# Kernel tuning notes

Hardware: AMD Instinct MI355X
Metric: run time of the kernel (lower is better)

## Reference

```python
import jax, jax.numpy as jnp
import numpy as np
from math import comb

N_VARS = 4

def _binom_vec(n):
    return jnp.asarray([comb(n, i) for i in range(n + 1)], dtype=jnp.float32)

def _conv_ind(L):
    M = np.zeros((L, L, 2 * L - 1), dtype=np.float32)
    for i in range(L):
        for j in range(L):
            M[i, j, i + j] = 1.0
    return jnp.asarray(M)

def _elev(d, D):
    # Bernstein degree-elevation matrix (d+1, D+1)
    E = np.zeros((d + 1, D + 1), dtype=np.float32)
    for k in range(D + 1):
        for i in range(d + 1):
            if 0 <= k - i <= D - d:
                E[i, k] = comb(d, i) * comb(D - d, k - i) / comb(D, k)
    return jnp.asarray(E)

def _mult_const(p, c):
    # multiply implicit-Bernstein poly (T, n, L) by scalar c: scale variable-0 rows
    return jnp.concatenate([p[:, :1, :] * c, p[:, 1:, :]], axis=1)

def _const_term(c, n, L):
    return _mult_const(jnp.ones((1, n, L), dtype=jnp.float32), c)

def _square_poly(p):
    # Bernstein product of p with itself: (T,n,L) -> (T*T, n, 2L-1)
    T, n, L = p.shape
    w = p * _binom_vec(L - 1)
    conv = jnp.einsum('avi,bvj,ijk->abvk', w, w, _conv_ind(L))
    return (conv / _binom_vec(2 * L - 2)).reshape(T * T, n, 2 * L - 1)

def _ibf_minmax(p):
    # interval bound of IBF poly: per-row min/max, interval product over vars, sum over terms
    lo = p.min(axis=2); hi = p.max(axis=2)  # (T, n)
    L_, U_ = lo[:, 0], hi[:, 0]
    for v in range(1, p.shape[1]):
        c = jnp.stack([L_ * lo[:, v], L_ * hi[:, v], U_ * lo[:, v], U_ * hi[:, v]])
        L_, U_ = c.min(axis=0), c.max(axis=0)
    return L_.sum(), U_.sum()

def _quad_of_poly(p, coeffs):
    # a*p^2 + b*p + c in implicit Bernstein form; degree doubles
    T, n, L = p.shape
    a, b, c = coeffs[0], coeffs[1], coeffs[2]
    p2 = _mult_const(_square_poly(p), a)
    bp = jnp.einsum('tvi,ik->tvk', _mult_const(p, b), _elev(L - 1, 2 * L - 2))
    return jnp.concatenate([p2, bp, _const_term(c, n, 2 * L - 1)], axis=0)

def _combine(inputs, weights):
    # sum_k w_k * P_k: scale each poly's var-0 rows by w_k, concatenate terms
    s = jnp.concatenate([inputs[:, :, :1, :] * weights[:, None, None, None],
                         inputs[:, :, 1:, :]], axis=2)
    K, T, n, L = s.shape
    return s.reshape(K * T, n, L)

def setup_inputs():
    key = jax.random.key(0)
    ks = jax.random.split(key, 5)
    K, T, n, L = 32, 16, N_VARS, 4
    return {
        'layer_inputs_under': 0.1 * jax.random.normal(ks[0], (K, T * n, L), jnp.float32),
        'layer_inputs_over': 0.1 * jax.random.normal(ks[1], (K, T * n, L), jnp.float32),
        'layer_inputs_under_degrees': jnp.full((K, n), L - 1, jnp.int32),
        'layer_inputs_over_degrees': jnp.full((K, n), L - 1, jnp.int32),
        'node_pos_weights': jax.random.normal(ks[2], (K,), jnp.float32),
        'node_neg_weights': jax.random.normal(ks[3], (K,), jnp.float32),
        'node_bias': 0.1 * jax.random.normal(ks[4], (1,), jnp.float32),
    }

def reference(layer_inputs_under, layer_inputs_over, layer_inputs_under_degrees,
              layer_inputs_over_degrees, node_pos_weights, node_neg_weights, node_bias):
    n = N_VARS
    K, TN, L = layer_inputs_under.shape
    T = TN // n
    iu = layer_inputs_under.reshape(K, T, n, L)
    io = layer_inputs_over.reshape(K, T, n, L)
    bias = node_bias[0]
    under = jnp.concatenate([_combine(io, node_neg_weights),
                             _combine(iu, node_pos_weights),
                             _const_term(bias, n, L)], axis=0)
    over = jnp.concatenate([_combine(io, node_pos_weights),
                            _combine(iu, node_neg_weights),
                            _const_term(bias, n, L)], axis=0)
    deg = jnp.maximum(layer_inputs_under_degrees.max(axis=0),
                      layer_inputs_over_degrees.max(axis=0)).astype(jnp.float32)
    l = _ibf_minmax(under)[0]
    u = _ibf_minmax(over)[1]
    lf, uf = float(l), float(u)
    L2 = 2 * L - 1
    if uf <= 0.0:  # node always inactive
        z = jnp.zeros((1,), jnp.float32)
        return z, z, jnp.zeros(n, jnp.float32), jnp.zeros(n, jnp.float32)
    if lf >= 0.0:  # node always active -> identity
        return under.reshape(-1, L), over.reshape(-1, L), deg, deg
    # l < 0 < u: quadratic ReLU relaxation (degree doubles)
    # under: (x^2 - l*x)/(u-l) <= relu(x); over: u*(x-l)^2/(u-l)^2 >= relu(x)
    cu = jnp.stack([1.0 / (u - l), -l / (u - l), jnp.zeros_like(u)])
    co = jnp.stack([u / (u - l) ** 2, -2.0 * u * l / (u - l) ** 2, u * l ** 2 / (u - l) ** 2])
    ru = _quad_of_poly(under, cu)
    ro = _quad_of_poly(over, co)
    return ru.reshape(-1, L2), ro.reshape(-1, L2), 2.0 * deg, 2.0 * deg
```

## Files before the change

### kernel.cpp

```cpp
#include <hip/hip_runtime.h>

static constexpr int       KT    = 512;
static constexpr int       TROWS = 1025;
static constexpr long long PAIRS = 1050625LL;
static constexpr long long ROWSO = 1051651LL;
static constexpr long long RUF   = ROWSO * 28;
static constexpr int       NB    = 4105;
static constexpr int       NTAIL = 5;

static constexpr int WS_UNDER = 0;
static constexpr int WS_OVER  = TROWS * 16;
static constexpr int WS_SCAL  = 2 * TROWS * 16;

__device__ __forceinline__ void row_interval(const float q[16], float& Lr, float& Ur)
{
    float L_ = fminf(fminf(q[0], q[1]), fminf(q[2], q[3]));
    float U_ = fmaxf(fmaxf(q[0], q[1]), fmaxf(q[2], q[3]));
#pragma unroll
    for (int v = 1; v < 4; ++v) {
        const float a0 = q[4*v+0], a1 = q[4*v+1], a2 = q[4*v+2], a3 = q[4*v+3];
        const float lo = fminf(fminf(a0, a1), fminf(a2, a3));
        const float hi = fmaxf(fmaxf(a0, a1), fmaxf(a2, a3));
        const float c0 = L_*lo, c1 = L_*hi, c2 = U_*lo, c3 = U_*hi;
        L_ = fminf(fminf(c0, c1), fminf(c2, c3));
        U_ = fmaxf(fmaxf(c0, c1), fmaxf(c2, c3));
    }
    Lr = L_; Ur = U_;
}

__global__ __launch_bounds__(1024)
void phaseA(const float* __restrict__ iu, const float* __restrict__ io,
            const float* __restrict__ posw, const float* __restrict__ negw,
            const float* __restrict__ biasp, float* __restrict__ ws)
{
    __shared__ float sl[16];
    __shared__ float su[16];
    const int t = threadIdx.x;
    const float bias = biasp[0];

    const float* src = (t < KT) ? io : iu;
    const int s  = (t < KT) ? t : t - KT;
    const int k  = s >> 4;

    const float4* rp = (const float4*)(src + s * 16);
    const float4 r0 = rp[0], r1 = rp[1], r2 = rp[2], r3 = rp[3];
    const float p[16] = { r0.x, r0.y, r0.z, r0.w, r1.x, r1.y, r1.z, r1.w,
                          r2.x, r2.y, r2.z, r2.w, r3.x, r3.y, r3.z, r3.w };

    const float wU = (t < KT) ? negw[k] : posw[k];
    const float wO = (t < KT) ? posw[k] : negw[k];

    float un[16], ov[16];
#pragma unroll
    for (int i = 0; i < 16; ++i) {
        const float sU = (i < 4) ? wU : 1.0f;
        const float sO = (i < 4) ? wO : 1.0f;
        un[i] = p[i] * sU;
        ov[i] = p[i] * sO;
    }
    float4* wu4 = (float4*)(ws + WS_UNDER + t * 16);
    float4* wo4 = (float4*)(ws + WS_OVER  + t * 16);
#pragma unroll
    for (int i = 0; i < 4; ++i) {
        wu4[i] = make_float4(un[4*i], un[4*i+1], un[4*i+2], un[4*i+3]);
        wo4[i] = make_float4(ov[4*i], ov[4*i+1], ov[4*i+2], ov[4*i+3]);
    }

    float Lu, Uu, Lo, Uo;
    row_interval(un, Lu, Uu);
    row_interval(ov, Lo, Uo);
    float accL = Lu;
    float accU = Uo;
#pragma unroll
    for (int off = 32; off > 0; off >>= 1) {
        accL += __shfl_down(accL, off, 64);
        accU += __shfl_down(accU, off, 64);
    }
    if ((t & 63) == 0) { sl[t >> 6] = accL; su[t >> 6] = accU; }
    __syncthreads();
    if (t == 0) {
#pragma unroll
        for (int i = 0; i < 16; ++i) {
            const float cv = (i < 4) ? bias : 1.0f;
            ws[WS_UNDER + 1024 * 16 + i] = cv;
            ws[WS_OVER  + 1024 * 16 + i] = cv;
        }
        float l = bias, u = bias;
#pragma unroll
        for (int w = 0; w < 16; ++w) { l += sl[w]; u += su[w]; }
        const float d    = u - l;
        const float inv  = 1.0f / d;
        const float inv2 = inv * inv;
        ws[WS_SCAL + 0] = inv;
        ws[WS_SCAL + 1] = -l * inv;
        ws[WS_SCAL + 2] = 0.0f;
        ws[WS_SCAL + 3] = u * inv2;
        ws[WS_SCAL + 4] = -2.0f * u * l * inv2;
        ws[WS_SCAL + 5] = u * l * l * inv2;
    }
}

__global__ __launch_bounds__(256)
void phaseBC(const float* __restrict__ ws,
             const int* __restrict__ degu, const int* __restrict__ dego,
             float* __restrict__ out)
{
    __shared__ float lds[256 * 29];
    const int t   = threadIdx.x;
    const int bx  = blockIdx.x;
    const int sel = blockIdx.y;
    float* outT = out + (long long)sel * RUF;

    if (bx >= NB) {
        const int id2 = (bx - NB) * 256 + t;
        const float B = ws[WS_SCAL + sel * 3 + 1];
        const float C = ws[WS_SCAL + sel * 3 + 2];
        if (id2 <= TROWS) {
            float o[28];
            if (id2 < TROWS) {
                const float* P = ws + sel * WS_OVER + id2 * 16;
#pragma unroll
                for (int v = 0; v < 4; ++v) {
                    const float sB = (v == 0) ? B : 1.0f;
                    const float q0 = P[4*v+0]*sB, q1 = P[4*v+1]*sB;
                    const float q2 = P[4*v+2]*sB, q3 = P[4*v+3]*sB;
                    o[7*v+0] = q0;
                    o[7*v+1] = 0.5f*(q0 + q1);
                    o[7*v+2] = 0.2f*q0 + 0.6f*q1 + 0.2f*q2;
                    o[7*v+3] = 0.05f*q0 + 0.45f*q1 + 0.45f*q2 + 0.05f*q3;
                    o[7*v+4] = 0.2f*q1 + 0.6f*q2 + 0.2f*q3;
                    o[7*v+5] = 0.5f*(q2 + q3);
                    o[7*v+6] = q3;
                }
            } else {
#pragma unroll
                for (int j = 0; j < 28; ++j) o[j] = (j < 7) ? C : 1.0f;
            }
            float* dst = outT + (PAIRS + (long long)id2) * 28LL;
#pragma unroll
            for (int j = 0; j < 28; ++j) dst[j] = o[j];
        } else if (sel == 0 && id2 >= TROWS + 1 && id2 < TROWS + 9) {
            const int j = id2 - (TROWS + 1);
            const int v = j & 3;
            int m = 0;
            for (int kk = 0; kk < 32; ++kk)
                m = max(m, max(degu[kk * 4 + v], dego[kk * 4 + v]));
            out[2 * RUF + j] = 2.0f * (float)m;
        }
        return;
    }

    const long long blockPair = (long long)bx * 256;
    const long long idx = blockPair + t;

    const float* P = ws + sel * WS_OVER;
    const float  A = ws[WS_SCAL + sel * 3];

    if (idx < PAIRS) {
        const unsigned r = (unsigned)idx;
        const unsigned a = r / 1025u;
        const unsigned b = r - a * 1025u;
        const float* pa = P + a * 16;
        const float* pb = P + b * 16;

        float o[28];
#pragma unroll
        for (int v = 0; v < 4; ++v) {
            const float wa0 = pa[4*v+0],       wa1 = pa[4*v+1] * 3.f;
            const float wa2 = pa[4*v+2] * 3.f, wa3 = pa[4*v+3];
            const float wb0 = pb[4*v+0],       wb1 = pb[4*v+1] * 3.f;
            const float wb2 = pb[4*v+2] * 3.f, wb3 = pb[4*v+3];
            const float sA = (v == 0) ? A : 1.0f;
            o[7*v+0] = (wa0*wb0) * sA;
            o[7*v+1] = (wa0*wb1 + wa1*wb0) * (sA * (1.f/6.f));
            o[7*v+2] = (wa0*wb2 + wa1*wb1 + wa2*wb0) * (sA * (1.f/15.f));
            o[7*v+3] = (wa0*wb3 + wa1*wb2 + wa2*wb1 + wa3*wb0) * (sA * 0.05f);
            o[7*v+4] = (wa1*wb3 + wa2*wb2 + wa3*wb1) * (sA * (1.f/15.f));
            o[7*v+5] = (wa2*wb3 + wa3*wb2) * (sA * (1.f/6.f));
            o[7*v+6] = (wa3*wb3) * sA;
        }
#pragma unroll
        for (int j = 0; j < 28; ++j) lds[t * 29 + j] = o[j];
    }
    __syncthreads();

    const long long totalChunks = PAIRS * 7;
#pragma unroll
    for (int it = 0; it < 7; ++it) {
        const int local = it * 256 + t;
        const long long c = blockPair * 7 + local;
        if (c < totalChunks) {
            const int p = local / 7;
            const int q = local - p * 7;
            float4 vv;
            vv.x = lds[p * 29 + q * 4 + 0];
            vv.y = lds[p * 29 + q * 4 + 1];
            vv.z = lds[p * 29 + q * 4 + 2];
            vv.w = lds[p * 29 + q * 4 + 3];
            ((float4*)outT)[c] = vv;
        }
    }
}

extern "C" void kernel_launch(void* const* d_in, const int* in_sizes, int n_in,
                              void* d_out, int out_size, void* d_ws, size_t ws_size,
                              hipStream_t stream)
{
    const float* iu   = (const float*)d_in[0];
    const float* io   = (const float*)d_in[1];
    const int*   degu = (const int*)d_in[2];
    const int*   dego = (const int*)d_in[3];
    const float* posw = (const float*)d_in[4];
    const float* negw = (const float*)d_in[5];
    const float* bias = (const float*)d_in[6];
    float* out = (float*)d_out;
    float* ws  = (float*)d_ws;

    hipLaunchKernelGGL(phaseA, dim3(1), dim3(1024), 0, stream,
                       iu, io, posw, negw, bias, ws);

    hipLaunchKernelGGL(phaseBC, dim3(NB + NTAIL, 2), dim3(256), 0, stream,
                       ws, degu, dego, out);
}
```

Baseline: 48.12 us.

## Halve LDS staging buffer and split pair compute into two half-block passes

The main phaseBC path now stages only 128 pairs at a time in shared memory, so the LDS array shrinks by half. Each block runs two passes: half the threads compute products into LDS, then all threads store float4 chunks. Inputs are now read as float4, the per-variable loop is kept rolled to cut register use, and launch_bounds requests 8 blocks per CU, all aimed at higher occupancy. The cost is that half the threads sit idle during each compute pass, and there are four barriers per block instead of one.

```diff
diff --git a/kernel.cpp b/kernel.cpp
--- a/kernel.cpp
+++ b/kernel.cpp
@@ -100,12 +100,12 @@
     }
 }
 
-__global__ __launch_bounds__(256)
+__global__ __launch_bounds__(256, 8)
 void phaseBC(const float* __restrict__ ws,
              const int* __restrict__ degu, const int* __restrict__ dego,
              float* __restrict__ out)
 {
-    __shared__ float lds[256 * 29];
+    __shared__ float lds[128 * 29];
     const int t   = threadIdx.x;
     const int bx  = blockIdx.x;
     const int sel = blockIdx.y;
@@ -150,55 +150,60 @@
         return;
     }
 
-    const long long blockPair = (long long)bx * 256;
-    const long long idx = blockPair + t;
-
+    const long long blockPair   = (long long)bx * 256;
+    const long long bp7         = blockPair * 7;
+    const long long totalChunks = PAIRS * 7;
     const float* P = ws + sel * WS_OVER;
     const float  A = ws[WS_SCAL + sel * 3];
 
-    if (idx < PAIRS) {
-        const unsigned r = (unsigned)idx;
-        const unsigned a = r / 1025u;
-        const unsigned b = r - a * 1025u;
-        const float* pa = P + a * 16;
-        const float* pb = P + b * 16;
-
-        float o[28];
-#pragma unroll
-        for (int v = 0; v < 4; ++v) {
-            const float wa0 = pa[4*v+0],       wa1 = pa[4*v+1] * 3.f;
-            const float wa2 = pa[4*v+2] * 3.f, wa3 = pa[4*v+3];
-            const float wb0 = pb[4*v+0],       wb1 = pb[4*v+1] * 3.f;
-            const float wb2 = pb[4*v+2] * 3.f, wb3 = pb[4*v+3];
-            const float sA = (v == 0) ? A : 1.0f;
-            o[7*v+0] = (wa0*wb0) * sA;
-            o[7*v+1] = (wa0*wb1 + wa1*wb0) * (sA * (1.f/6.f));
-            o[7*v+2] = (wa0*wb2 + wa1*wb1 + wa2*wb0) * (sA * (1.f/15.f));
-            o[7*v+3] = (wa0*wb3 + wa1*wb2 + wa2*wb1 + wa3*wb0) * (sA * 0.05f);
-            o[7*v+4] = (wa1*wb3 + wa2*wb2 + wa3*wb1) * (sA * (1.f/15.f));
-            o[7*v+5] = (wa2*wb3 + wa3*wb2) * (sA * (1.f/6.f));
-            o[7*v+6] = (wa3*wb3) * sA;
-        }
-#pragma unroll
-        for (int j = 0; j < 28; ++j) lds[t * 29 + j] = o[j];
-    }
-    __syncthreads();
-
-    const long long totalChunks = PAIRS * 7;
-#pragma unroll
-    for (int it = 0; it < 7; ++it) {
-        const int local = it * 256 + t;
-        const long long c = blockPair * 7 + local;
-        if (c < totalChunks) {
-            const int p = local / 7;
-            const int q = local - p * 7;
-            float4 vv;
-            vv.x = lds[p * 29 + q * 4 + 0];
-            vv.y = lds[p * 29 + q * 4 + 1];
-            vv.z = lds[p * 29 + q * 4 + 2];
-            vv.w = lds[p * 29 + q * 4 + 3];
-            ((float4*)outT)[c] = vv;
-        }
+    for (int h = 0; h < 2; ++h) {
+        const int tl = t & 127;
+        if ((t >> 7) == h) {
+            const long long idx = blockPair + (long long)h * 128 + tl;
+            if (idx < PAIRS) {
+                const unsigned r = (unsigned)idx;
+                const unsigned a = r / 1025u;
+                const unsigned b = r - a * 1025u;
+                const float4* pa = (const float4*)(P + a * 16);
+                const float4* pb = (const float4*)(P + b * 16);
+#pragma unroll 1
+                for (int v = 0; v < 4; ++v) {
+                    const float4 av = pa[v];
+                    const float4 bv = pb[v];
+                    const float wa0 = av.x, wa1 = av.y * 3.f;
+                    const float wa2 = av.z * 3.f, wa3 = av.w;
+                    const float wb0 = bv.x, wb1 = bv.y * 3.f;
+                    const float wb2 = bv.z * 3.f, wb3 = bv.w;
+                    const float sA = (v == 0) ? A : 1.0f;
+                    float* Lp = &lds[tl * 29 + v * 7];
+                    Lp[0] = (wa0*wb0) * sA;
+                    Lp[1] = (wa0*wb1 + wa1*wb0) * (sA * (1.f/6.f));
+                    Lp[2] = (wa0*wb2 + wa1*wb1 + wa2*wb0) * (sA * (1.f/15.f));
+                    Lp[3] = (wa0*wb3 + wa1*wb2 + wa2*wb1 + wa3*wb0) * (sA * 0.05f);
+                    Lp[4] = (wa1*wb3 + wa2*wb2 + wa3*wb1) * (sA * (1.f/15.f));
+                    Lp[5] = (wa2*wb3 + wa3*wb2) * (sA * (1.f/6.f));
+                    Lp[6] = (wa3*wb3) * sA;
+                }
+            }
+        }
+        __syncthreads();
+
+#pragma unroll
+        for (int it = 0; it < 4; ++it) {
+            const int local = it * 256 + t;
+            const long long c = bp7 + (long long)h * 896 + local;
+            if (local < 896 && c < totalChunks) {
+                const int p = local / 7;
+                const int q = local - p * 7;
+                float4 vv;
+                vv.x = lds[p * 29 + q * 4 + 0];
+                vv.y = lds[p * 29 + q * 4 + 1];
+                vv.z = lds[p * 29 + q * 4 + 2];
+                vv.w = lds[p * 29 + q * 4 + 3];
+                ((float4*)outT)[c] = vv;
+            }
+        }
+        __syncthreads();
     }
 }
 
```

Measured after the change: 48.43 us. About the same (+0.6%).

## Compute square-product chunks directly per output float4, dropping LDS staging

Applied to the files above, without the earlier changes.

The pair-product kernel no longer computes 28 outputs per thread and transposes them through LDS. Each thread now computes one float4 output chunk directly from four float4 loads of pre-scaled rows, with the quadratic coefficient split as a square root into each factor and the binomial weights folded in ahead of time. The linear-term tail reads the raw inputs itself, so phase A no longer writes a separate scaled copy for it. This removes the LDS round trip and barrier, but adds redundant arithmetic and select chains per chunk, and sqrt of A may be NaN if A is negative.

```diff
diff --git a/kernel.cpp b/kernel.cpp
--- a/kernel.cpp
+++ b/kernel.cpp
@@ -1,16 +1,17 @@
 #include <hip/hip_runtime.h>
 
-static constexpr int       KT    = 512;
-static constexpr int       TROWS = 1025;
-static constexpr long long PAIRS = 1050625LL;
-static constexpr long long ROWSO = 1051651LL;
-static constexpr long long RUF   = ROWSO * 28;
-static constexpr int       NB    = 4105;
-static constexpr int       NTAIL = 5;
-
-static constexpr int WS_UNDER = 0;
-static constexpr int WS_OVER  = TROWS * 16;
-static constexpr int WS_SCAL  = 2 * TROWS * 16;
+static constexpr int       KT     = 512;
+static constexpr int       TROWS  = 1025;
+static constexpr long long PAIRS  = 1050625LL;
+static constexpr long long ROWSO  = 1051651LL;
+static constexpr long long RUF    = ROWSO * 28;
+static constexpr long long CHUNKS = PAIRS * 7;
+static constexpr int       NB     = 4105;
+static constexpr int       NTAIL  = 5;
+
+static constexpr int WS_SQ_U = 0;
+static constexpr int WS_SQ_O = TROWS * 16;
+static constexpr int WS_SCAL = 2 * TROWS * 16;
 
 __device__ __forceinline__ void row_interval(const float q[16], float& Lr, float& Ur)
 {
@@ -33,8 +34,7 @@
             const float* __restrict__ posw, const float* __restrict__ negw,
             const float* __restrict__ biasp, float* __restrict__ ws)
 {
-    __shared__ float sl[16];
-    __shared__ float su[16];
+    __shared__ float sl[16], su[16], sA[2];
     const int t = threadIdx.x;
     const float bias = biasp[0];
 
@@ -58,13 +58,6 @@
         un[i] = p[i] * sU;
         ov[i] = p[i] * sO;
     }
-    float4* wu4 = (float4*)(ws + WS_UNDER + t * 16);
-    float4* wo4 = (float4*)(ws + WS_OVER  + t * 16);
-#pragma unroll
-    for (int i = 0; i < 4; ++i) {
-        wu4[i] = make_float4(un[4*i], un[4*i+1], un[4*i+2], un[4*i+3]);
-        wo4[i] = make_float4(ov[4*i], ov[4*i+1], ov[4*i+2], ov[4*i+3]);
-    }
 
     float Lu, Uu, Lo, Uo;
     row_interval(un, Lu, Uu);
@@ -79,33 +72,55 @@
     if ((t & 63) == 0) { sl[t >> 6] = accL; su[t >> 6] = accU; }
     __syncthreads();
     if (t == 0) {
-#pragma unroll
-        for (int i = 0; i < 16; ++i) {
-            const float cv = (i < 4) ? bias : 1.0f;
-            ws[WS_UNDER + 1024 * 16 + i] = cv;
-            ws[WS_OVER  + 1024 * 16 + i] = cv;
-        }
         float l = bias, u = bias;
 #pragma unroll
         for (int w = 0; w < 16; ++w) { l += sl[w]; u += su[w]; }
         const float d    = u - l;
         const float inv  = 1.0f / d;
         const float inv2 = inv * inv;
-        ws[WS_SCAL + 0] = inv;
-        ws[WS_SCAL + 1] = -l * inv;
-        ws[WS_SCAL + 2] = 0.0f;
-        ws[WS_SCAL + 3] = u * inv2;
-        ws[WS_SCAL + 4] = -2.0f * u * l * inv2;
-        ws[WS_SCAL + 5] = u * l * l * inv2;
+        const float A_u  = inv;
+        const float A_o  = u * inv2;
+        ws[WS_SCAL + 0] = -l * inv;
+        ws[WS_SCAL + 1] = 0.0f;
+        ws[WS_SCAL + 2] = -2.0f * u * l * inv2;
+        ws[WS_SCAL + 3] = u * l * l * inv2;
+        sA[0] = sqrtf(A_u);
+        sA[1] = sqrtf(A_o);
+    }
+    __syncthreads();
+    const float qU = sA[0], qO = sA[1];
+
+    float4* du = (float4*)(ws + WS_SQ_U + t * 16);
+    float4* dov= (float4*)(ws + WS_SQ_O + t * 16);
+#pragma unroll
+    for (int v = 0; v < 4; ++v) {
+        const float mU = (v == 0) ? qU : 1.0f;
+        const float mO = (v == 0) ? qO : 1.0f;
+        du[v]  = make_float4(un[4*v]*mU, 3.f*un[4*v+1]*mU, 3.f*un[4*v+2]*mU, un[4*v+3]*mU);
+        dov[v] = make_float4(ov[4*v]*mO, 3.f*ov[4*v+1]*mO, 3.f*ov[4*v+2]*mO, ov[4*v+3]*mO);
+    }
+    if (t == 0) {
+        float4* cu4 = (float4*)(ws + WS_SQ_U + 1024 * 16);
+        float4* co4 = (float4*)(ws + WS_SQ_O + 1024 * 16);
+#pragma unroll
+        for (int v = 0; v < 4; ++v) {
+            const float base = (v == 0) ? bias : 1.0f;
+            const float mU = (v == 0) ? qU : 1.0f;
+            const float mO = (v == 0) ? qO : 1.0f;
+            cu4[v] = make_float4(base*mU, 3.f*base*mU, 3.f*base*mU, base*mU);
+            co4[v] = make_float4(base*mO, 3.f*base*mO, 3.f*base*mO, base*mO);
+        }
     }
 }
 
 __global__ __launch_bounds__(256)
 void phaseBC(const float* __restrict__ ws,
              const int* __restrict__ degu, const int* __restrict__ dego,
+             const float* __restrict__ posw, const float* __restrict__ negw,
+             const float* __restrict__ biasp,
+             const float* __restrict__ iu, const float* __restrict__ io,
              float* __restrict__ out)
 {
-    __shared__ float lds[256 * 29];
     const int t   = threadIdx.x;
     const int bx  = blockIdx.x;
     const int sel = blockIdx.y;
@@ -113,17 +128,38 @@
 
     if (bx >= NB) {
         const int id2 = (bx - NB) * 256 + t;
-        const float B = ws[WS_SCAL + sel * 3 + 1];
-        const float C = ws[WS_SCAL + sel * 3 + 2];
+        const float B = ws[WS_SCAL + sel * 2 + 0];
+        const float C = ws[WS_SCAL + sel * 2 + 1];
         if (id2 <= TROWS) {
             float o[28];
             if (id2 < TROWS) {
-                const float* P = ws + sel * WS_OVER + id2 * 16;
+                float raw[16];
+                float w;
+                if (id2 < 1024) {
+                    const float* src = (id2 < KT) ? io : iu;
+                    const int s2 = (id2 < KT) ? id2 : id2 - KT;
+                    const int k2 = s2 >> 4;
+                    const float4* rp = (const float4*)(src + s2 * 16);
+#pragma unroll
+                    for (int v = 0; v < 4; ++v) {
+                        const float4 rv = rp[v];
+                        raw[4*v+0] = rv.x; raw[4*v+1] = rv.y;
+                        raw[4*v+2] = rv.z; raw[4*v+3] = rv.w;
+                    }
+                    const bool isIo = (id2 < KT);
+                    w = (sel == 0) ? (isIo ? negw[k2] : posw[k2])
+                                   : (isIo ? posw[k2] : negw[k2]);
+                } else {
+                    const float bias = biasp[0];
+#pragma unroll
+                    for (int i = 0; i < 16; ++i) raw[i] = (i < 4) ? bias : 1.0f;
+                    w = 1.0f;
+                }
 #pragma unroll
                 for (int v = 0; v < 4; ++v) {
-                    const float sB = (v == 0) ? B : 1.0f;
-                    const float q0 = P[4*v+0]*sB, q1 = P[4*v+1]*sB;
-                    const float q2 = P[4*v+2]*sB, q3 = P[4*v+3]*sB;
+                    const float sB = (v == 0) ? w * B : 1.0f;
+                    const float q0 = raw[4*v+0]*sB, q1 = raw[4*v+1]*sB;
+                    const float q2 = raw[4*v+2]*sB, q3 = raw[4*v+3]*sB;
                     o[7*v+0] = q0;
                     o[7*v+1] = 0.5f*(q0 + q1);
                     o[7*v+2] = 0.2f*q0 + 0.6f*q1 + 0.2f*q2;
@@ -150,54 +186,56 @@
         return;
     }
 
-    const long long blockPair = (long long)bx * 256;
-    const long long idx = blockPair + t;
-
-    const float* P = ws + sel * WS_OVER;
-    const float  A = ws[WS_SCAL + sel * 3];
-
-    if (idx < PAIRS) {
-        const unsigned r = (unsigned)idx;
-        const unsigned a = r / 1025u;
-        const unsigned b = r - a * 1025u;
-        const float* pa = P + a * 16;
-        const float* pb = P + b * 16;
-
-        float o[28];
-#pragma unroll
-        for (int v = 0; v < 4; ++v) {
-            const float wa0 = pa[4*v+0],       wa1 = pa[4*v+1] * 3.f;
-            const float wa2 = pa[4*v+2] * 3.f, wa3 = pa[4*v+3];
-            const float wb0 = pb[4*v+0],       wb1 = pb[4*v+1] * 3.f;
-            const float wb2 = pb[4*v+2] * 3.f, wb3 = pb[4*v+3];
-            const float sA = (v == 0) ? A : 1.0f;
-            o[7*v+0] = (wa0*wb0) * sA;
-            o[7*v+1] = (wa0*wb1 + wa1*wb0) * (sA * (1.f/6.f));
-            o[7*v+2] = (wa0*wb2 + wa1*wb1 + wa2*wb0) * (sA * (1.f/15.f));
-            o[7*v+3] = (wa0*wb3 + wa1*wb2 + wa2*wb1 + wa3*wb0) * (sA * 0.05f);
-            o[7*v+4] = (wa1*wb3 + wa2*wb2 + wa3*wb1) * (sA * (1.f/15.f));
-            o[7*v+5] = (wa2*wb3 + wa3*wb2) * (sA * (1.f/6.f));
-            o[7*v+6] = (wa3*wb3) * sA;
-        }
-#pragma unroll
-        for (int j = 0; j < 28; ++j) lds[t * 29 + j] = o[j];
-    }
-    __syncthreads();
-
-    const long long totalChunks = PAIRS * 7;
+    const float4* SQ = (const float4*)(ws + sel * WS_SQ_O);
+    const long long cbase = (long long)bx * 1792;
+
 #pragma unroll
     for (int it = 0; it < 7; ++it) {
-        const int local = it * 256 + t;
-        const long long c = blockPair * 7 + local;
-        if (c < totalChunks) {
-            const int p = local / 7;
-            const int q = local - p * 7;
-            float4 vv;
-            vv.x = lds[p * 29 + q * 4 + 0];
-            vv.y = lds[p * 29 + q * 4 + 1];
-            vv.z = lds[p * 29 + q * 4 + 2];
-            vv.w = lds[p * 29 + q * 4 + 3];
-            ((float4*)outT)[c] = vv;
+        const long long c = cbase + it * 256 + t;
+        if (c < CHUNKS) {
+            const unsigned cc = (unsigned)c;
+            const unsigned r  = cc / 7u;
+            const int      q  = (int)(cc - r * 7u);
+            const unsigned a  = r / 1025u;
+            const unsigned b  = r - a * 1025u;
+
+            const int vA = q >> 1;
+            const int o  = (q & 1) ? (vA + 4) : vA;
+            const int vB = (vA < 3) ? vA + 1 : 3;
+
+            const float4 fa = SQ[a * 4 + vA];
+            const float4 fb = SQ[b * 4 + vA];
+            const float4 ga = SQ[a * 4 + vB];
+            const float4 gb = SQ[b * 4 + vB];
+
+            const float l0 = fa.x*fb.x;
+            const float l1 = (fa.x*fb.y + fa.y*fb.x) * (1.f/6.f);
+            const float l2 = (fa.x*fb.z + fa.y*fb.y + fa.z*fb.x) * (1.f/15.f);
+            const float l3 = (fa.x*fb.w + fa.y*fb.z + fa.z*fb.y + fa.w*fb.x) * 0.05f;
+            const float l4 = (fa.y*fb.w + fa.z*fb.z + fa.w*fb.y) * (1.f/15.f);
+            const float l5 = (fa.z*fb.w + fa.w*fb.z) * (1.f/6.f);
+            const float l6 = fa.w*fb.w;
+            const float h0 = ga.x*gb.x;
+            const float h1 = (ga.x*gb.y + ga.y*gb.x) * (1.f/6.f);
+            const float h2 = (ga.x*gb.z + ga.y*gb.y + ga.z*gb.x) * (1.f/15.f);
+
+            float rr[4];
+#pragma unroll
+            for (int e = 0; e < 4; ++e) {
+                const int kk = o + e;
+                float x = l0;
+                x = (kk == 1) ? l1 : x;
+                x = (kk == 2) ? l2 : x;
+                x = (kk == 3) ? l3 : x;
+                x = (kk == 4) ? l4 : x;
+                x = (kk == 5) ? l5 : x;
+                x = (kk == 6) ? l6 : x;
+                x = (kk == 7) ? h0 : x;
+                x = (kk == 8) ? h1 : x;
+                x = (kk == 9) ? h2 : x;
+                rr[e] = x;
+            }
+            ((float4*)outT)[c] = make_float4(rr[0], rr[1], rr[2], rr[3]);
         }
     }
 }
@@ -220,5 +258,5 @@
                        iu, io, posw, negw, bias, ws);
 
     hipLaunchKernelGGL(phaseBC, dim3(NB + NTAIL, 2), dim3(256), 0, stream,
-                       ws, degu, dego, out);
-}
+                       ws, degu, dego, posw, negw, bias, iu, io, out);
+}
```

New measurement: 60.69 us. 1.26x slower.
